# Kernel optimization log

Hardware: AMD Instinct MI355X
Metric: run time of the kernel (lower is better)

Reference implementation:

```python
import jax, jax.numpy as jnp
import numpy as np

B, N, D, C, H = 16384, 32, 256, 128, 8
LEAKY_ALPHA = 0.2  # tf.nn.leaky_relu default


def setup_inputs() -> dict:
    key = jax.random.key(0)
    k1, k2, k3, k4 = jax.random.split(key, 4)
    return {
        "node_feats": jax.random.normal(k1, (B, D), dtype=jnp.float32),
        "neighbors_feats": jax.random.normal(k2, (B, N, D), dtype=jnp.float32),
        "kernel": jax.random.normal(k3, (D, C), dtype=jnp.float32) * 0.05,
        "attn_kernel": jax.random.normal(k4, (1, H, 2 * C), dtype=jnp.float32) * 0.05,
        "attn_bias": jnp.zeros((H * C,), dtype=jnp.float32),
    }


def reference(node_feats, neighbors_feats, kernel, attn_kernel, attn_bias):
    # Project node and neighbor features: [B,C], [B,N,C]
    node_p = jnp.einsum('bd,dc->bc', node_feats, kernel)
    neigh_p = jnp.einsum('bnd,dc->bnc', neighbors_feats, kernel)
    # attn_kernel [1,H,2C]: split instead of materializing tile+concat [B,N,2C]
    a = attn_kernel[0]                 # [H, 2C]
    a_src, a_dst = a[:, :C], a[:, C:]  # each [H, C]
    # score[b,n,h] = concat(node_p[b], neigh_p[b,n]) . a[h]
    scores = (jnp.einsum('bc,hc->bh', node_p, a_src)[:, None, :]
              + jnp.einsum('bnc,hc->bnh', neigh_p, a_dst))  # [B,N,H]
    scores = jnp.transpose(scores, (0, 2, 1))  # [B,H,N]
    coef = jax.nn.softmax(jax.nn.leaky_relu(scores, LEAKY_ALPHA), axis=-1)
    # dropout is identity at inference (Keras default training=False)
    z = jnp.einsum('bhn,bnc->bhc', coef, neigh_p)  # [B,H,C]
    z = z.reshape(B, H * C) + attn_bias            # concat heads + bias
    return z[None, ...]  # [1,B,H*C]
```

## Files before the change

kernel.cpp:

```cpp
#include <hip/hip_runtime.h>

#define BB 16384
#define NN 32
#define DD 256
#define CC 128
#define HH 8
#define ALPHA 0.2f

#define SA_STRIDE 264
#define SP_STRIDE 48

typedef __attribute__((ext_vector_type(8))) short bf16x8;
typedef __attribute__((ext_vector_type(4))) float f32x4;

__device__ __forceinline__ unsigned short f2b(float x) {
    unsigned int u = __float_as_uint(x);
    return (unsigned short)((u + 0x7fffu + ((u >> 16) & 1u)) >> 16);
}
__device__ __forceinline__ uint2 pack4(float a, float b, float c, float d) {
    uint2 r;
    r.x = (unsigned)f2b(a) | ((unsigned)f2b(b) << 16);
    r.y = (unsigned)f2b(c) | ((unsigned)f2b(d) << 16);
    return r;
}

__global__ __launch_bounds__(256) void prep_kernel(const float* __restrict__ kern,
                                                   const float* __restrict__ attn,
                                                   unsigned short* __restrict__ kfrag,
                                                   unsigned short* __restrict__ sfrag) {
    if (blockIdx.x < 16) {
        int tid = blockIdx.x * 256 + threadIdx.x;
        int nt   = tid >> 9;
        int ks   = (tid >> 6) & 7;
        int lane = tid & 63;
        int q    = lane >> 4;
        int cc   = lane & 15;
        int c    = nt * 16 + cc;
        unsigned short v[8];
#pragma unroll
        for (int j = 0; j < 8; ++j) {
            int k = ks * 32 + q * 8 + j;
            v[j] = f2b(kern[k * CC + c]);
        }
        uint4* dst = (uint4*)(kfrag + ((size_t)(nt * 8 + ks) * 64 + lane) * 8);
        uint4 pk;
        pk.x = (unsigned)v[0] | ((unsigned)v[1] << 16);
        pk.y = (unsigned)v[2] | ((unsigned)v[3] << 16);
        pk.z = (unsigned)v[4] | ((unsigned)v[5] << 16);
        pk.w = (unsigned)v[6] | ((unsigned)v[7] << 16);
        *dst = pk;
    } else {
        int sid = (blockIdx.x - 16) * 256 + threadIdx.x;
        int ks   = sid >> 6;
        int lane = sid & 63;
        int q    = lane >> 4;
        int cc   = lane & 15;
        unsigned short v[8];
#pragma unroll
        for (int j = 0; j < 8; ++j) {
            int k = ks * 32 + q * 8 + j;
            const float* krow = kern + (size_t)k * CC;
            const float* arow = (cc < 8) ? (attn + cc * (2 * CC) + CC)
                                         : (attn + (cc - 8) * (2 * CC));
            float s0 = 0.f, s1 = 0.f;
#pragma unroll 4
            for (int c = 0; c < CC; c += 2) {
                s0 += krow[c] * arow[c];
                s1 += krow[c + 1] * arow[c + 1];
            }
            v[j] = f2b(s0 + s1);
        }
        uint4* dst = (uint4*)(sfrag + ((size_t)ks * 64 + lane) * 8);
        uint4 pk;
        pk.x = (unsigned)v[0] | ((unsigned)v[1] << 16);
        pk.y = (unsigned)v[2] | ((unsigned)v[3] << 16);
        pk.z = (unsigned)v[4] | ((unsigned)v[5] << 16);
        pk.w = (unsigned)v[6] | ((unsigned)v[7] << 16);
        *dst = pk;
    }
}

__global__ __launch_bounds__(256, 4) void gat_kernel(const float* __restrict__ node,
                                                     const float* __restrict__ neigh,
                                                     const float* __restrict__ bias,
                                                     const unsigned short* __restrict__ kfrag,
                                                     const unsigned short* __restrict__ sfrag,
                                                     float* __restrict__ out) {
    const int b    = blockIdx.x;
    const int t    = threadIdx.x;
    const int lane = t & 63;
    const int wave = t >> 6;
    const int q    = lane >> 4;
    const int m15  = lane & 15;

    __shared__ __align__(16) char smem[39712];
    unsigned short* sA    = (unsigned short*)smem;
    unsigned short* sP    = (unsigned short*)(smem + 25344);
    unsigned short* cfrag = (unsigned short*)(smem + 37632);
    float*          sDst  = (float*)(smem + 38656);
    float*          sSrc  = (float*)(smem + 39680);

    {
        const float4* nb4 = (const float4*)(neigh + (size_t)b * (NN * DD));
        const float4* nd4 = (const float4*)(node + (size_t)b * DD);
        for (int j = t; j < 33 * 64; j += 256) {
            int row = j >> 6, d4 = j & 63;
            float4 v = (row < 32) ? nb4[row * 64 + d4] : nd4[d4];
            *(uint2*)(sA + row * SA_STRIDE + d4 * 4) = pack4(v.x, v.y, v.z, v.w);
        }
    }
    __syncthreads();

    if (wave < 3) {
        const int mt = wave;
        f32x4 acc = {0.f, 0.f, 0.f, 0.f};
        const unsigned short* abase = sA + (mt * 16 + m15) * SA_STRIDE + q * 8;
#pragma unroll
        for (int ks = 0; ks < 8; ++ks) {
            bf16x8 bfr = *(const bf16x8*)(sfrag + ((size_t)ks * 64 + lane) * 8);
            bf16x8 afr = *(const bf16x8*)(abase + ks * 32);
            acc = __builtin_amdgcn_mfma_f32_16x16x32_bf16(afr, bfr, acc, 0, 0, 0);
        }
#pragma unroll
        for (int r = 0; r < 4; ++r) {
            int row = mt * 16 + q * 4 + r;
            if (row < 32 && m15 < 8) sDst[row * 8 + m15] = acc[r];
            if (row == 32 && m15 >= 8) sSrc[m15 - 8] = acc[r];
        }
    }

#pragma unroll
    for (int nti = 0; nti < 2; ++nti) {
        const int nt = wave * 2 + nti;
        bf16x8 kb[8];
#pragma unroll
        for (int ks = 0; ks < 8; ++ks)
            kb[ks] = *(const bf16x8*)(kfrag + ((size_t)(nt * 8 + ks) * 64 + lane) * 8);
#pragma unroll
        for (int mt = 0; mt < 2; ++mt) {
            f32x4 acc = {0.f, 0.f, 0.f, 0.f};
            const unsigned short* abase = sA + (mt * 16 + m15) * SA_STRIDE + q * 8;
#pragma unroll
            for (int ks = 0; ks < 8; ++ks) {
                bf16x8 afr = *(const bf16x8*)(abase + ks * 32);
                acc = __builtin_amdgcn_mfma_f32_16x16x32_bf16(afr, kb[ks], acc, 0, 0, 0);
            }
            int c  = nt * 16 + m15;
            int n0 = mt * 16 + q * 4;
            *(uint2*)(sP + c * SP_STRIDE + n0) = pack4(acc[0], acc[1], acc[2], acc[3]);
        }
    }
    __syncthreads();

    {
        int h = t >> 5, n = t & 31;
        float sc = sSrc[h] + sDst[n * 8 + h];
        sc = fmaxf(sc, ALPHA * sc);
        float m = sc;
#pragma unroll
        for (int off = 16; off >= 1; off >>= 1) m = fmaxf(m, __shfl_xor(m, off, 32));
        float e = expf(sc - m);
        float den = e;
#pragma unroll
        for (int off = 16; off >= 1; off >>= 1) den += __shfl_xor(den, off, 32);
        float coef = e / den;
        int l1 = (n >> 3) * 16 + h;
        int jj = n & 7;
        cfrag[l1 * 8 + jj] = f2b(coef);
        cfrag[(l1 + 8) * 8 + jj] = 0;
    }
    __syncthreads();

    {
        bf16x8 cb = *(const bf16x8*)(cfrag + (size_t)lane * 8);
        f32x4 zero = {0.f, 0.f, 0.f, 0.f};
#pragma unroll
        for (int i = 0; i < 2; ++i) {
            int mt5 = wave * 2 + i;
            bf16x8 afr = *(const bf16x8*)(sP + (mt5 * 16 + m15) * SP_STRIDE + q * 8);
            f32x4 acc = __builtin_amdgcn_mfma_f32_16x16x32_bf16(afr, cb, zero, 0, 0, 0);
            if (m15 < 8) {
                int h  = m15;
                int c0 = mt5 * 16 + q * 4;
                float4 bv = *(const float4*)(bias + h * CC + c0);
                float4 r;
                r.x = acc[0] + bv.x;
                r.y = acc[1] + bv.y;
                r.z = acc[2] + bv.z;
                r.w = acc[3] + bv.w;
                *(float4*)(out + (size_t)b * (HH * CC) + h * CC + c0) = r;
            }
        }
    }
}

extern "C" void kernel_launch(void* const* d_in, const int* in_sizes, int n_in,
                              void* d_out, int out_size, void* d_ws, size_t ws_size,
                              hipStream_t stream) {
    const float* node  = (const float*)d_in[0];
    const float* neigh = (const float*)d_in[1];
    const float* kern  = (const float*)d_in[2];
    const float* attn  = (const float*)d_in[3];
    const float* bias  = (const float*)d_in[4];
    float* out = (float*)d_out;

    unsigned short* kfrag = (unsigned short*)d_ws;
    unsigned short* sfrag = (unsigned short*)((char*)d_ws + 65536);

    hipLaunchKernelGGL(prep_kernel, dim3(18), dim3(256), 0, stream, kern, attn, kfrag, sfrag);
    hipLaunchKernelGGL(gat_kernel, dim3(BB), dim3(256), 0, stream,
                       node, neigh, bias, kfrag, sfrag, out);
}
```

Measured before the change: 793.4 us.

## Make GAT kernel persistent with register-prefetched double-buffered node loads

Replaces the one-block-per-node grid with a persistent grid of 768 blocks that loop over nodes. While the current node is computed from one LDS buffer, the next node's neighbor features are prefetched into registers and written into a second buffer. Projection weight fragments are loaded into registers once per block instead of once per node. The intent is to hide global-load latency and remove per-block launch and weight-reload overhead, at the cost of more LDS and registers per block, which lowers occupancy (launch bounds go from 4 to 3 blocks per SM).

```diff
diff --git a/kernel.cpp b/kernel.cpp
--- a/kernel.cpp
+++ b/kernel.cpp
@@ -6,8 +6,10 @@
 #define CC 128
 #define HH 8
 #define ALPHA 0.2f
+#define GRID 768
 
 #define SA_STRIDE 264
+#define SA_BUF    8712
 #define SP_STRIDE 48
 
 typedef __attribute__((ext_vector_type(8))) short bf16x8;
@@ -80,118 +82,163 @@
     }
 }
 
-__global__ __launch_bounds__(256, 4) void gat_kernel(const float* __restrict__ node,
+__global__ __launch_bounds__(256, 3) void gat_kernel(const float* __restrict__ node,
                                                      const float* __restrict__ neigh,
                                                      const float* __restrict__ bias,
                                                      const unsigned short* __restrict__ kfrag,
                                                      const unsigned short* __restrict__ sfrag,
                                                      float* __restrict__ out) {
-    const int b    = blockIdx.x;
     const int t    = threadIdx.x;
     const int lane = t & 63;
     const int wave = t >> 6;
     const int q    = lane >> 4;
     const int m15  = lane & 15;
 
-    __shared__ __align__(16) char smem[39712];
-    unsigned short* sA    = (unsigned short*)smem;
-    unsigned short* sP    = (unsigned short*)(smem + 25344);
-    unsigned short* cfrag = (unsigned short*)(smem + 37632);
-    float*          sDst  = (float*)(smem + 38656);
-    float*          sSrc  = (float*)(smem + 39680);
-
-    {
-        const float4* nb4 = (const float4*)(neigh + (size_t)b * (NN * DD));
-        const float4* nd4 = (const float4*)(node + (size_t)b * DD);
-        for (int j = t; j < 33 * 64; j += 256) {
-            int row = j >> 6, d4 = j & 63;
-            float4 v = (row < 32) ? nb4[row * 64 + d4] : nd4[d4];
-            *(uint2*)(sA + row * SA_STRIDE + d4 * 4) = pack4(v.x, v.y, v.z, v.w);
-        }
-    }
+    __shared__ __align__(16) char smem[49216];
+    unsigned short* sAb   = (unsigned short*)smem;
+    unsigned short* sP    = (unsigned short*)(smem + 34848);
+    unsigned short* cfrag = (unsigned short*)(smem + 47136);
+    float*          sDst  = (float*)(smem + 48160);
+    float*          sSrc  = (float*)(smem + 49184);
+
+    bf16x8 kb[2][8];
+#pragma unroll
+    for (int i = 0; i < 2; ++i)
+#pragma unroll
+        for (int ks = 0; ks < 8; ++ks)
+            kb[i][ks] = *(const bf16x8*)(kfrag + ((size_t)((wave * 2 + i) * 8 + ks) * 64 + lane) * 8);
+
+    const float4* nb4 = (const float4*)neigh;
+    const float4* nd4 = (const float4*)node;
+
+    float4 st[9];
+
+#define LOAD_NODE(bb)                                                          \
+    {                                                                          \
+        _Pragma("unroll")                                                      \
+        for (int k = 0; k < 9; ++k) {                                          \
+            int j = k * 256 + t;                                               \
+            if (j < 33 * 64) {                                                 \
+                int row = j >> 6, d4 = j & 63;                                 \
+                st[k] = (row < 32) ? nb4[(size_t)(bb) * 2048 + row * 64 + d4]  \
+                                   : nd4[(size_t)(bb) * 64 + d4];              \
+            }                                                                  \
+        }                                                                      \
+    }
+
+#define WRITE_NODE(buf)                                                        \
+    {                                                                          \
+        unsigned short* sAw = sAb + (buf) * SA_BUF;                            \
+        _Pragma("unroll")                                                      \
+        for (int k = 0; k < 9; ++k) {                                          \
+            int j = k * 256 + t;                                               \
+            if (j < 33 * 64) {                                                 \
+                int row = j >> 6, d4 = j & 63;                                 \
+                *(uint2*)(sAw + row * SA_STRIDE + d4 * 4) =                    \
+                    pack4(st[k].x, st[k].y, st[k].z, st[k].w);                 \
+            }                                                                  \
+        }                                                                      \
+    }
+
+    int b = blockIdx.x;
+    LOAD_NODE(b);
+    WRITE_NODE(0);
     __syncthreads();
-
-    if (wave < 3) {
-        const int mt = wave;
-        f32x4 acc = {0.f, 0.f, 0.f, 0.f};
-        const unsigned short* abase = sA + (mt * 16 + m15) * SA_STRIDE + q * 8;
-#pragma unroll
-        for (int ks = 0; ks < 8; ++ks) {
-            bf16x8 bfr = *(const bf16x8*)(sfrag + ((size_t)ks * 64 + lane) * 8);
-            bf16x8 afr = *(const bf16x8*)(abase + ks * 32);
-            acc = __builtin_amdgcn_mfma_f32_16x16x32_bf16(afr, bfr, acc, 0, 0, 0);
-        }
-#pragma unroll
-        for (int r = 0; r < 4; ++r) {
-            int row = mt * 16 + q * 4 + r;
-            if (row < 32 && m15 < 8) sDst[row * 8 + m15] = acc[r];
-            if (row == 32 && m15 >= 8) sSrc[m15 - 8] = acc[r];
-        }
-    }
-
-#pragma unroll
-    for (int nti = 0; nti < 2; ++nti) {
-        const int nt = wave * 2 + nti;
-        bf16x8 kb[8];
-#pragma unroll
-        for (int ks = 0; ks < 8; ++ks)
-            kb[ks] = *(const bf16x8*)(kfrag + ((size_t)(nt * 8 + ks) * 64 + lane) * 8);
+    int cur = 0;
+
+    while (true) {
+        const int  bn   = b + GRID;
+        const bool more = (bn < BB);
+        if (more) LOAD_NODE(bn);
+
+        const unsigned short* sA = sAb + cur * SA_BUF;
+
+        if (wave < 3) {
+            f32x4 acc = {0.f, 0.f, 0.f, 0.f};
+            const unsigned short* abase = sA + (wave * 16 + m15) * SA_STRIDE + q * 8;
+#pragma unroll
+            for (int ks = 0; ks < 8; ++ks) {
+                bf16x8 bfr = *(const bf16x8*)(sfrag + ((size_t)ks * 64 + lane) * 8);
+                bf16x8 afr = *(const bf16x8*)(abase + ks * 32);
+                acc = __builtin_amdgcn_mfma_f32_16x16x32_bf16(afr, bfr, acc, 0, 0, 0);
+            }
+#pragma unroll
+            for (int r = 0; r < 4; ++r) {
+                int row = wave * 16 + q * 4 + r;
+                if (row < 32 && m15 < 8) sDst[row * 8 + m15] = acc[r];
+                if (row == 32 && m15 >= 8) sSrc[m15 - 8] = acc[r];
+            }
+        }
+
 #pragma unroll
         for (int mt = 0; mt < 2; ++mt) {
-            f32x4 acc = {0.f, 0.f, 0.f, 0.f};
+            bf16x8 afr[8];
             const unsigned short* abase = sA + (mt * 16 + m15) * SA_STRIDE + q * 8;
 #pragma unroll
-            for (int ks = 0; ks < 8; ++ks) {
-                bf16x8 afr = *(const bf16x8*)(abase + ks * 32);
-                acc = __builtin_amdgcn_mfma_f32_16x16x32_bf16(afr, kb[ks], acc, 0, 0, 0);
-            }
-            int c  = nt * 16 + m15;
-            int n0 = mt * 16 + q * 4;
-            *(uint2*)(sP + c * SP_STRIDE + n0) = pack4(acc[0], acc[1], acc[2], acc[3]);
-        }
-    }
-    __syncthreads();
-
-    {
-        int h = t >> 5, n = t & 31;
-        float sc = sSrc[h] + sDst[n * 8 + h];
-        sc = fmaxf(sc, ALPHA * sc);
-        float m = sc;
-#pragma unroll
-        for (int off = 16; off >= 1; off >>= 1) m = fmaxf(m, __shfl_xor(m, off, 32));
-        float e = expf(sc - m);
-        float den = e;
-#pragma unroll
-        for (int off = 16; off >= 1; off >>= 1) den += __shfl_xor(den, off, 32);
-        float coef = e / den;
-        int l1 = (n >> 3) * 16 + h;
-        int jj = n & 7;
-        cfrag[l1 * 8 + jj] = f2b(coef);
-        cfrag[(l1 + 8) * 8 + jj] = 0;
-    }
-    __syncthreads();
-
-    {
-        bf16x8 cb = *(const bf16x8*)(cfrag + (size_t)lane * 8);
-        f32x4 zero = {0.f, 0.f, 0.f, 0.f};
-#pragma unroll
-        for (int i = 0; i < 2; ++i) {
-            int mt5 = wave * 2 + i;
-            bf16x8 afr = *(const bf16x8*)(sP + (mt5 * 16 + m15) * SP_STRIDE + q * 8);
-            f32x4 acc = __builtin_amdgcn_mfma_f32_16x16x32_bf16(afr, cb, zero, 0, 0, 0);
-            if (m15 < 8) {
-                int h  = m15;
-                int c0 = mt5 * 16 + q * 4;
-                float4 bv = *(const float4*)(bias + h * CC + c0);
-                float4 r;
-                r.x = acc[0] + bv.x;
-                r.y = acc[1] + bv.y;
-                r.z = acc[2] + bv.z;
-                r.w = acc[3] + bv.w;
-                *(float4*)(out + (size_t)b * (HH * CC) + h * CC + c0) = r;
-            }
-        }
-    }
+            for (int ks = 0; ks < 8; ++ks)
+                afr[ks] = *(const bf16x8*)(abase + ks * 32);
+#pragma unroll
+            for (int i = 0; i < 2; ++i) {
+                f32x4 acc = {0.f, 0.f, 0.f, 0.f};
+#pragma unroll
+                for (int ks = 0; ks < 8; ++ks)
+                    acc = __builtin_amdgcn_mfma_f32_16x16x32_bf16(afr[ks], kb[i][ks], acc, 0, 0, 0);
+                int c  = (wave * 2 + i) * 16 + m15;
+                int n0 = mt * 16 + q * 4;
+                *(uint2*)(sP + c * SP_STRIDE + n0) = pack4(acc[0], acc[1], acc[2], acc[3]);
+            }
+        }
+        __syncthreads();
+
+        {
+            int h = t >> 5, n = t & 31;
+            float sc = sSrc[h] + sDst[n * 8 + h];
+            sc = fmaxf(sc, ALPHA * sc);
+            float m = sc;
+#pragma unroll
+            for (int off = 16; off >= 1; off >>= 1) m = fmaxf(m, __shfl_xor(m, off, 32));
+            float e = expf(sc - m);
+            float den = e;
+#pragma unroll
+            for (int off = 16; off >= 1; off >>= 1) den += __shfl_xor(den, off, 32);
+            float coef = e / den;
+            int l1 = (n >> 3) * 16 + h;
+            int jj = n & 7;
+            cfrag[l1 * 8 + jj] = f2b(coef);
+            cfrag[(l1 + 8) * 8 + jj] = 0;
+        }
+        __syncthreads();
+
+        {
+            bf16x8 cb = *(const bf16x8*)(cfrag + (size_t)lane * 8);
+            f32x4 zero = {0.f, 0.f, 0.f, 0.f};
+#pragma unroll
+            for (int i = 0; i < 2; ++i) {
+                int mt5 = wave * 2 + i;
+                bf16x8 afr = *(const bf16x8*)(sP + (mt5 * 16 + m15) * SP_STRIDE + q * 8);
+                f32x4 acc = __builtin_amdgcn_mfma_f32_16x16x32_bf16(afr, cb, zero, 0, 0, 0);
+                if (m15 < 8) {
+                    int h  = m15;
+                    int c0 = mt5 * 16 + q * 4;
+                    float4 bv = *(const float4*)(bias + h * CC + c0);
+                    float4 r;
+                    r.x = acc[0] + bv.x;
+                    r.y = acc[1] + bv.y;
+                    r.z = acc[2] + bv.z;
+                    r.w = acc[3] + bv.w;
+                    *(float4*)(out + (size_t)b * (HH * CC) + h * CC + c0) = r;
+                }
+            }
+        }
+
+        if (!more) break;
+        WRITE_NODE(cur ^ 1);
+        __syncthreads();
+        cur ^= 1;
+        b = bn;
+    }
+#undef LOAD_NODE
+#undef WRITE_NODE
 }
 
 extern "C" void kernel_launch(void* const* d_in, const int* in_sizes, int n_in,
@@ -208,6 +255,6 @@
     unsigned short* sfrag = (unsigned short*)((char*)d_ws + 65536);
 
     hipLaunchKernelGGL(prep_kernel, dim3(18), dim3(256), 0, stream, kern, attn, kfrag, sfrag);
-    hipLaunchKernelGGL(gat_kernel, dim3(BB), dim3(256), 0, stream,
+    hipLaunchKernelGGL(gat_kernel, dim3(GRID), dim3(256), 0, stream,
                        node, neigh, bias, kfrag, sfrag, out);
 }
```

New measurement: 1.056 ms. 1.33x slower.
